# Kernel tuning notes

Hardware: AMD Instinct MI355X
Metric: run time of the kernel (lower is better)

Reference implementation:

```python
import jax, jax.numpy as jnp
import numpy as np

F_NODES = 16384   # number of function nodes
DEG = 8           # in-degree == out-degree per function node
E = F_NODES * DEG # edge-latent dimension (num edges)
B = 64            # batch
H = 16            # hidden_channels of each per-node MLP
LAYERS = 10       # GSNN layers (weights shared across layers)


def setup_inputs() -> dict:
    key = jax.random.key(0)
    k0, k1, k2, k3 = jax.random.split(key, 4)
    x0 = jax.random.normal(k0, (B, E), dtype=jnp.float32)
    # each edge has exactly one destination function node -> in_ixs is a permutation of edges
    in_ixs = jax.random.permutation(k1, E).reshape(F_NODES, DEG)
    # per-node 2-layer MLP weights: in_degree -> H -> out_degree
    W1 = jax.random.normal(k2, (F_NODES, H, DEG), dtype=jnp.float32) * (1.0 / np.sqrt(DEG))
    b1 = jnp.zeros((F_NODES, H), dtype=jnp.float32)
    W2 = jax.random.normal(k3, (F_NODES, DEG, H), dtype=jnp.float32) * (1.0 / np.sqrt(H))
    b2 = jnp.zeros((F_NODES, DEG), dtype=jnp.float32)
    return {"x0": x0, "W1": W1, "b1": b1, "W2": W2, "b2": b2, "in_ixs": in_ixs}


def reference(x0, W1, b1, W2, b2, in_ixs):
    # x0: [B, E] edge-latent input. Each layer: every function node gathers its
    # in-edges, applies its own small MLP, scatters to its out-edges; results are
    # summed into x_new and a residual x0 is added (GSNN.forward).
    x = x0
    for _ in range(LAYERS):
        g = x[:, in_ixs]                                   # [B, F, DEG] gather in-edge values
        h = jax.nn.elu(jnp.einsum('bfd,fhd->bfh', g, W1) + b1)  # [B, F, H]
        o = jnp.einsum('bfh,foh->bfo', h, W2) + b2         # [B, F, DEG]
        # out-edges of node f are the contiguous slots f*DEG:(f+1)*DEG (disjoint scatter)
        x = o.reshape(x0.shape) + x0                       # sum of node scatters + residual
    return x
```

## Files before the change

### kernel.cpp

```cpp
#include <hip/hip_runtime.h>
#include <math.h>

#define F_NODES 16384
#define DEG 8
#define E_TOT (F_NODES * DEG)
#define B 64
#define H 16
#define LAYERS 10

__global__ __launch_bounds__(256) void transpose_in_kernel(
    const float* __restrict__ x0, float* __restrict__ xT)
{
    __shared__ float tile[64 * 65];
    const int e0 = blockIdx.x * 64;
    const int c  = threadIdx.x & 63;
    const int r  = threadIdx.x >> 6;

    #pragma unroll
    for (int i = 0; i < 16; ++i) {
        const int b = r + i * 4;
        tile[c * 65 + b] = x0[(size_t)b * E_TOT + e0 + c];
    }
    __syncthreads();
    const int b = threadIdx.x & 63;
    #pragma unroll
    for (int i = 0; i < 16; ++i) {
        const int el = r + i * 4;
        xT[(size_t)(e0 + el) * B + b] = tile[el * 65 + b];
    }
}

__device__ __forceinline__ float fast_elu(float x)
{
    float e = __builtin_amdgcn_exp2f(x * 1.44269504088896340736f) - 1.0f;
    return x > 0.0f ? x : e;
}

#define NPW 2

template <bool FINAL>
__global__ __launch_bounds__(256) void layer_kernel(
    const float* __restrict__ xin,
    const float* __restrict__ x0T,
    const float* __restrict__ W1,
    const float* __restrict__ b1,
    const float* __restrict__ W2,
    const float* __restrict__ b2,
    const int*   __restrict__ in_ixs,
    float* __restrict__ xout)
{
    const int lane    = threadIdx.x & 63;
    const int wv      = threadIdx.x >> 6;
    const int wave_id = (int)blockIdx.x * 4 + wv;

    #pragma unroll
    for (int n = 0; n < NPW; ++n) {
        const int f = __builtin_amdgcn_readfirstlane(wave_id * NPW + n);

        const int* ixp = in_ixs + f * DEG;
        float g[DEG], r[DEG];
        const float* resp = x0T + (size_t)f * DEG * B + lane;
        #pragma unroll
        for (int d = 0; d < DEG; ++d) {
            const int ix = ixp[d];
            g[d] = xin[(size_t)ix * B + lane];
            r[d] = resp[d * B];
        }

        const float* w1  = W1 + f * (H * DEG);
        const float* bb1 = b1 + f * H;
        float h[H];
        #pragma unroll
        for (int j = 0; j < H; ++j) {
            float acc = bb1[j];
            #pragma unroll
            for (int d = 0; d < DEG; ++d)
                acc = fmaf(w1[j * DEG + d], g[d], acc);
            h[j] = fast_elu(acc);
        }

        const float* w2  = W2 + f * (DEG * H);
        const float* bb2 = b2 + f * DEG;
        float o[DEG];
        #pragma unroll
        for (int d = 0; d < DEG; ++d) {
            float acc = bb2[d];
            #pragma unroll
            for (int j = 0; j < H; ++j)
                acc = fmaf(w2[d * H + j], h[j], acc);
            o[d] = acc + r[d];
        }

        if (FINAL) {
            float4 v0 = make_float4(o[0], o[1], o[2], o[3]);
            float4 v1 = make_float4(o[4], o[5], o[6], o[7]);
            float4* dst = (float4*)(xout + (size_t)lane * E_TOT + f * DEG);
            dst[0] = v0;
            dst[1] = v1;
        } else {
            float* outp = xout + (size_t)f * DEG * B + lane;
            #pragma unroll
            for (int d = 0; d < DEG; ++d)
                outp[d * B] = o[d];
        }
    }
}

extern "C" void kernel_launch(void* const* d_in, const int* in_sizes, int n_in,
                              void* d_out, int out_size, void* d_ws, size_t ws_size,
                              hipStream_t stream)
{
    const float* x0     = (const float*)d_in[0];
    const float* W1     = (const float*)d_in[1];
    const float* b1     = (const float*)d_in[2];
    const float* W2     = (const float*)d_in[3];
    const float* b2     = (const float*)d_in[4];
    const int*   in_ixs = (const int*)d_in[5];
    float* out = (float*)d_out;

    const size_t NEL = (size_t)E_TOT * B;
    float* buf0 = (float*)d_ws;
    float* buf1 = buf0 + NEL;
    float* buf2 = buf1 + NEL;

    transpose_in_kernel<<<E_TOT / 64, 256, 0, stream>>>(x0, buf0);

    const int grid = F_NODES / (4 * NPW);
    const float* cur = buf0;
    float* nxt = buf1;
    for (int l = 0; l < LAYERS; ++l) {
        if (l == LAYERS - 1) {
            layer_kernel<true><<<grid, 256, 0, stream>>>(
                cur, buf0, W1, b1, W2, b2, in_ixs, out);
        } else {
            layer_kernel<false><<<grid, 256, 0, stream>>>(
                cur, buf0, W1, b1, W2, b2, in_ixs, nxt);
            cur = nxt;
            nxt = (cur == buf1) ? buf2 : buf1;
        }
    }
}
```

Before: 359.4 us.

## Store intermediate layers in consumer order so reads become sequential

Builds an inverse permutation of in_ixs once per call. Every non-final layer then scatters each node's outputs to the slots where their consuming node will read them. Later layers can read their inputs contiguously instead of through an index-dependent gather, which takes the dependent index load and the random reads off the load critical path. The random access moves to the stores, which do not stall the wave. It adds a small extra kernel and extra workspace for the inverse index array.

```diff
diff --git a/kernel.cpp b/kernel.cpp
--- a/kernel.cpp
+++ b/kernel.cpp
@@ -30,6 +30,13 @@
     }
 }
 
+__global__ __launch_bounds__(256) void build_inv_kernel(
+    const int* __restrict__ in_ixs, int* __restrict__ inv)
+{
+    const int k = blockIdx.x * 256 + threadIdx.x;
+    inv[in_ixs[k]] = k;
+}
+
 __device__ __forceinline__ float fast_elu(float x)
 {
     float e = __builtin_amdgcn_exp2f(x * 1.44269504088896340736f) - 1.0f;
@@ -38,7 +45,7 @@
 
 #define NPW 2
 
-template <bool FINAL>
+template <bool SEQ_IN, int OUT_MODE>
 __global__ __launch_bounds__(256) void layer_kernel(
     const float* __restrict__ xin,
     const float* __restrict__ x0T,
@@ -47,6 +54,7 @@
     const float* __restrict__ W2,
     const float* __restrict__ b2,
     const int*   __restrict__ in_ixs,
+    const int*   __restrict__ inv,
     float* __restrict__ xout)
 {
     const int lane    = threadIdx.x & 63;
@@ -57,14 +65,23 @@
     for (int n = 0; n < NPW; ++n) {
         const int f = __builtin_amdgcn_readfirstlane(wave_id * NPW + n);
 
-        const int* ixp = in_ixs + f * DEG;
         float g[DEG], r[DEG];
         const float* resp = x0T + (size_t)f * DEG * B + lane;
-        #pragma unroll
-        for (int d = 0; d < DEG; ++d) {
-            const int ix = ixp[d];
-            g[d] = xin[(size_t)ix * B + lane];
-            r[d] = resp[d * B];
+        if (SEQ_IN) {
+            const float* inp = xin + (size_t)f * DEG * B + lane;
+            #pragma unroll
+            for (int d = 0; d < DEG; ++d) {
+                g[d] = inp[d * B];
+                r[d] = resp[d * B];
+            }
+        } else {
+            const int* ixp = in_ixs + f * DEG;
+            #pragma unroll
+            for (int d = 0; d < DEG; ++d) {
+                const int ix = ixp[d];
+                g[d] = xin[(size_t)ix * B + lane];
+                r[d] = resp[d * B];
+            }
         }
 
         const float* w1  = W1 + f * (H * DEG);
@@ -91,17 +108,19 @@
             o[d] = acc + r[d];
         }
 
-        if (FINAL) {
+        if (OUT_MODE == 1) {
             float4 v0 = make_float4(o[0], o[1], o[2], o[3]);
             float4 v1 = make_float4(o[4], o[5], o[6], o[7]);
             float4* dst = (float4*)(xout + (size_t)lane * E_TOT + f * DEG);
             dst[0] = v0;
             dst[1] = v1;
         } else {
-            float* outp = xout + (size_t)f * DEG * B + lane;
+            const int* invp = inv + f * DEG;
             #pragma unroll
-            for (int d = 0; d < DEG; ++d)
-                outp[d * B] = o[d];
+            for (int d = 0; d < DEG; ++d) {
+                const int k = invp[d];
+                xout[(size_t)k * B + lane] = o[d];
+            }
         }
     }
 }
@@ -122,21 +141,25 @@
     float* buf0 = (float*)d_ws;
     float* buf1 = buf0 + NEL;
     float* buf2 = buf1 + NEL;
+    int*   inv  = (int*)(buf2 + NEL);
 
     transpose_in_kernel<<<E_TOT / 64, 256, 0, stream>>>(x0, buf0);
+    build_inv_kernel<<<E_TOT / 256, 256, 0, stream>>>(in_ixs, inv);
 
     const int grid = F_NODES / (4 * NPW);
-    const float* cur = buf0;
-    float* nxt = buf1;
-    for (int l = 0; l < LAYERS; ++l) {
-        if (l == LAYERS - 1) {
-            layer_kernel<true><<<grid, 256, 0, stream>>>(
-                cur, buf0, W1, b1, W2, b2, in_ixs, out);
-        } else {
-            layer_kernel<false><<<grid, 256, 0, stream>>>(
-                cur, buf0, W1, b1, W2, b2, in_ixs, nxt);
-            cur = nxt;
-            nxt = (cur == buf1) ? buf2 : buf1;
-        }
+
+    layer_kernel<false, 0><<<grid, 256, 0, stream>>>(
+        buf0, buf0, W1, b1, W2, b2, in_ixs, inv, buf1);
+
+    const float* cur = buf1;
+    float* nxt = buf2;
+    for (int l = 1; l < LAYERS - 1; ++l) {
+        layer_kernel<true, 0><<<grid, 256, 0, stream>>>(
+            cur, buf0, W1, b1, W2, b2, in_ixs, inv, nxt);
+        cur = nxt;
+        nxt = (cur == buf1) ? buf2 : buf1;
     }
+
+    layer_kernel<true, 1><<<grid, 256, 0, stream>>>(
+        cur, buf0, W1, b1, W2, b2, in_ixs, inv, out);
 }
```

Result: no change. 362.7 us (+0.9%).

## Fuse all layers into one cooperative kernel with scatter-side permutation and grid sync

Applied to the files above, without the earlier changes.

Replaces the ten per-layer launches with a single cooperative kernel of 256 blocks of 1024 threads. Layers are separated by grid-wide barriers. An inverse permutation of in_ixs is built up front, so each node scatters its outputs straight into the gather-order slots of the next layer and then reads its inputs contiguously. The residual x0 values are kept in registers across all layers. The costs are grid.sync overhead on each layer, scattered writes instead of scattered reads, and fewer resident waves (NPW=4 per wave) to hide latency.

```diff
diff --git a/kernel.cpp b/kernel.cpp
--- a/kernel.cpp
+++ b/kernel.cpp
@@ -1,5 +1,8 @@
 #include <hip/hip_runtime.h>
+#include <hip/hip_cooperative_groups.h>
 #include <math.h>
+
+namespace cg = cooperative_groups;
 
 #define F_NODES 16384
 #define DEG 8
@@ -7,6 +10,11 @@
 #define B 64
 #define H 16
 #define LAYERS 10
+
+#define NB  256
+#define TPB 1024
+#define NPB (F_NODES / NB)
+#define NPW (NPB / (TPB / 64))
 
 __global__ __launch_bounds__(256) void transpose_in_kernel(
     const float* __restrict__ x0, float* __restrict__ xT)
@@ -30,78 +38,115 @@
     }
 }
 
+__global__ __launch_bounds__(256) void build_inv_kernel(
+    const int* __restrict__ in_ixs, int* __restrict__ inv)
+{
+    const int k = blockIdx.x * 256 + threadIdx.x;
+    inv[in_ixs[k]] = k;
+}
+
 __device__ __forceinline__ float fast_elu(float x)
 {
     float e = __builtin_amdgcn_exp2f(x * 1.44269504088896340736f) - 1.0f;
     return x > 0.0f ? x : e;
 }
 
-#define NPW 2
-
-template <bool FINAL>
-__global__ __launch_bounds__(256) void layer_kernel(
-    const float* __restrict__ xin,
+__global__ __launch_bounds__(TPB, 4) void gsnn_fused(
     const float* __restrict__ x0T,
     const float* __restrict__ W1,
     const float* __restrict__ b1,
     const float* __restrict__ W2,
     const float* __restrict__ b2,
     const int*   __restrict__ in_ixs,
-    float* __restrict__ xout)
+    const int*   __restrict__ inv,
+    float* __restrict__ zA,
+    float* __restrict__ zB,
+    float* __restrict__ out)
 {
-    const int lane    = threadIdx.x & 63;
-    const int wv      = threadIdx.x >> 6;
-    const int wave_id = (int)blockIdx.x * 4 + wv;
+    cg::grid_group grid = cg::this_grid();
 
-    #pragma unroll
-    for (int n = 0; n < NPW; ++n) {
-        const int f = __builtin_amdgcn_readfirstlane(wave_id * NPW + n);
+    const int lane = threadIdx.x & 63;
+    const int wv   = threadIdx.x >> 6;
+    const int f0   = __builtin_amdgcn_readfirstlane(
+                        (int)blockIdx.x * NPB + wv * NPW);
 
-        const int* ixp = in_ixs + f * DEG;
-        float g[DEG], r[DEG];
-        const float* resp = x0T + (size_t)f * DEG * B + lane;
+    float r[NPW][DEG];
+    {
+        const float* rp = x0T + (size_t)f0 * DEG * B + lane;
         #pragma unroll
-        for (int d = 0; d < DEG; ++d) {
-            const int ix = ixp[d];
-            g[d] = xin[(size_t)ix * B + lane];
-            r[d] = resp[d * B];
+        for (int n = 0; n < NPW; ++n)
+            #pragma unroll
+            for (int d = 0; d < DEG; ++d)
+                r[n][d] = rp[(n * DEG + d) * B];
+    }
+
+    const float* zin  = nullptr;
+    float*       zout = zA;
+
+    for (int l = 0; l < LAYERS; ++l) {
+        float g[NPW][DEG];
+        if (l == 0) {
+            #pragma unroll
+            for (int n = 0; n < NPW; ++n) {
+                const int* ixp = in_ixs + (f0 + n) * DEG;
+                #pragma unroll
+                for (int d = 0; d < DEG; ++d)
+                    g[n][d] = x0T[(size_t)ixp[d] * B + lane];
+            }
+        } else {
+            const float* zp = zin + (size_t)f0 * DEG * B + lane;
+            #pragma unroll
+            for (int n = 0; n < NPW; ++n)
+                #pragma unroll
+                for (int d = 0; d < DEG; ++d)
+                    g[n][d] = zp[(n * DEG + d) * B];
         }
 
-        const float* w1  = W1 + f * (H * DEG);
-        const float* bb1 = b1 + f * H;
-        float h[H];
         #pragma unroll
-        for (int j = 0; j < H; ++j) {
-            float acc = bb1[j];
+        for (int n = 0; n < NPW; ++n) {
+            const int f = f0 + n;
+            const float* w1  = W1 + f * (H * DEG);
+            const float* bb1 = b1 + f * H;
+            float h[H];
             #pragma unroll
-            for (int d = 0; d < DEG; ++d)
-                acc = fmaf(w1[j * DEG + d], g[d], acc);
-            h[j] = fast_elu(acc);
+            for (int j = 0; j < H; ++j) {
+                float acc = bb1[j];
+                #pragma unroll
+                for (int d = 0; d < DEG; ++d)
+                    acc = fmaf(w1[j * DEG + d], g[n][d], acc);
+                h[j] = fast_elu(acc);
+            }
+
+            const float* w2  = W2 + f * (DEG * H);
+            const float* bb2 = b2 + f * DEG;
+            float o[DEG];
+            #pragma unroll
+            for (int d = 0; d < DEG; ++d) {
+                float acc = bb2[d];
+                #pragma unroll
+                for (int j = 0; j < H; ++j)
+                    acc = fmaf(w2[d * H + j], h[j], acc);
+                o[d] = acc + r[n][d];
+            }
+
+            if (l == LAYERS - 1) {
+                float4 v0 = make_float4(o[0], o[1], o[2], o[3]);
+                float4 v1 = make_float4(o[4], o[5], o[6], o[7]);
+                float4* dst = (float4*)(out + (size_t)lane * E_TOT + f * DEG);
+                dst[0] = v0;
+                dst[1] = v1;
+            } else {
+                const int* invp = inv + f * DEG;
+                #pragma unroll
+                for (int d = 0; d < DEG; ++d)
+                    zout[(size_t)invp[d] * B + lane] = o[d];
+            }
         }
 
-        const float* w2  = W2 + f * (DEG * H);
-        const float* bb2 = b2 + f * DEG;
-        float o[DEG];
-        #pragma unroll
-        for (int d = 0; d < DEG; ++d) {
-            float acc = bb2[d];
-            #pragma unroll
-            for (int j = 0; j < H; ++j)
-                acc = fmaf(w2[d * H + j], h[j], acc);
-            o[d] = acc + r[d];
-        }
-
-        if (FINAL) {
-            float4 v0 = make_float4(o[0], o[1], o[2], o[3]);
-            float4 v1 = make_float4(o[4], o[5], o[6], o[7]);
-            float4* dst = (float4*)(xout + (size_t)lane * E_TOT + f * DEG);
-            dst[0] = v0;
-            dst[1] = v1;
-        } else {
-            float* outp = xout + (size_t)f * DEG * B + lane;
-            #pragma unroll
-            for (int d = 0; d < DEG; ++d)
-                outp[d * B] = o[d];
+        if (l < LAYERS - 1) {
+            grid.sync();
+            zin  = zout;
+            zout = (zout == zA) ? zB : zA;
         }
     }
 }
@@ -120,23 +165,17 @@
 
     const size_t NEL = (size_t)E_TOT * B;
     float* buf0 = (float*)d_ws;
-    float* buf1 = buf0 + NEL;
-    float* buf2 = buf1 + NEL;
+    float* bufA = buf0 + NEL;
+    float* bufB = bufA + NEL;
+    int*   inv  = (int*)(bufB + NEL);
 
     transpose_in_kernel<<<E_TOT / 64, 256, 0, stream>>>(x0, buf0);
+    build_inv_kernel<<<E_TOT / 256, 256, 0, stream>>>(in_ixs, inv);
 
-    const int grid = F_NODES / (4 * NPW);
-    const float* cur = buf0;
-    float* nxt = buf1;
-    for (int l = 0; l < LAYERS; ++l) {
-        if (l == LAYERS - 1) {
-            layer_kernel<true><<<grid, 256, 0, stream>>>(
-                cur, buf0, W1, b1, W2, b2, in_ixs, out);
-        } else {
-            layer_kernel<false><<<grid, 256, 0, stream>>>(
-                cur, buf0, W1, b1, W2, b2, in_ixs, nxt);
-            cur = nxt;
-            nxt = (cur == buf1) ? buf2 : buf1;
-        }
-    }
+    void* args[] = {
+        (void*)&buf0, (void*)&W1, (void*)&b1, (void*)&W2, (void*)&b2,
+        (void*)&in_ixs, (void*)&inv, (void*)&bufA, (void*)&bufB, (void*)&out
+    };
+    hipLaunchCooperativeKernel((const void*)gsnn_fused,
+                               dim3(NB), dim3(TPB), args, 0, stream);
 }
```

Measured after the change: 738.4 us. 105% more time.

## Batch gathers for four nodes per wave upfront with nontemporal loads and stores

Applied to the files above, without the earlier changes.

Each wave now handles four function nodes and issues all gather and residual loads for them before any compute, raising memory-level parallelism. Blocks grow to 512 threads, with launch bounds that ask for at least four blocks resident. Activation loads and stores use nontemporal hints. The cost is higher register pressure from holding 64 gathered values per lane, which could lower occupancy or cause spills. The nontemporal hints may also hurt cache reuse of x0T and of the next layer's input.

```diff
diff --git a/kernel.cpp b/kernel.cpp
--- a/kernel.cpp
+++ b/kernel.cpp
@@ -7,6 +7,12 @@
 #define B 64
 #define H 16
 #define LAYERS 10
+
+#define WPB 8
+#define TPB (WPB * 64)
+#define NPW 4
+#define NODES_PER_BLOCK (WPB * NPW)
+#define GRID (F_NODES / NODES_PER_BLOCK)
 
 __global__ __launch_bounds__(256) void transpose_in_kernel(
     const float* __restrict__ x0, float* __restrict__ xT)
@@ -36,10 +42,8 @@
     return x > 0.0f ? x : e;
 }
 
-#define NPW 2
-
 template <bool FINAL>
-__global__ __launch_bounds__(256) void layer_kernel(
+__global__ __launch_bounds__(TPB, 4) void layer_kernel(
     const float* __restrict__ xin,
     const float* __restrict__ x0T,
     const float* __restrict__ W1,
@@ -49,24 +53,32 @@
     const int*   __restrict__ in_ixs,
     float* __restrict__ xout)
 {
-    const int lane    = threadIdx.x & 63;
-    const int wv      = threadIdx.x >> 6;
-    const int wave_id = (int)blockIdx.x * 4 + wv;
+    const int lane = threadIdx.x & 63;
+    const int wv   = threadIdx.x >> 6;
+    const int f0   = __builtin_amdgcn_readfirstlane(
+                        ((int)blockIdx.x * WPB + wv) * NPW);
+
+    float g[NPW][DEG];
+    float r[NPW][DEG];
+    #pragma unroll
+    for (int n = 0; n < NPW; ++n) {
+        const int* ixp = in_ixs + (f0 + n) * DEG;
+        #pragma unroll
+        for (int d = 0; d < DEG; ++d)
+            g[n][d] = __builtin_nontemporal_load(
+                          xin + (size_t)ixp[d] * B + lane);
+    }
+    #pragma unroll
+    for (int n = 0; n < NPW; ++n) {
+        const float* rp = x0T + (size_t)(f0 + n) * DEG * B + lane;
+        #pragma unroll
+        for (int d = 0; d < DEG; ++d)
+            r[n][d] = __builtin_nontemporal_load(rp + d * B);
+    }
 
     #pragma unroll
     for (int n = 0; n < NPW; ++n) {
-        const int f = __builtin_amdgcn_readfirstlane(wave_id * NPW + n);
-
-        const int* ixp = in_ixs + f * DEG;
-        float g[DEG], r[DEG];
-        const float* resp = x0T + (size_t)f * DEG * B + lane;
-        #pragma unroll
-        for (int d = 0; d < DEG; ++d) {
-            const int ix = ixp[d];
-            g[d] = xin[(size_t)ix * B + lane];
-            r[d] = resp[d * B];
-        }
-
+        const int f = f0 + n;
         const float* w1  = W1 + f * (H * DEG);
         const float* bb1 = b1 + f * H;
         float h[H];
@@ -75,7 +87,7 @@
             float acc = bb1[j];
             #pragma unroll
             for (int d = 0; d < DEG; ++d)
-                acc = fmaf(w1[j * DEG + d], g[d], acc);
+                acc = fmaf(w1[j * DEG + d], g[n][d], acc);
             h[j] = fast_elu(acc);
         }
 
@@ -88,7 +100,7 @@
             #pragma unroll
             for (int j = 0; j < H; ++j)
                 acc = fmaf(w2[d * H + j], h[j], acc);
-            o[d] = acc + r[d];
+            o[d] = acc + r[n][d];
         }
 
         if (FINAL) {
@@ -101,7 +113,7 @@
             float* outp = xout + (size_t)f * DEG * B + lane;
             #pragma unroll
             for (int d = 0; d < DEG; ++d)
-                outp[d * B] = o[d];
+                __builtin_nontemporal_store(o[d], outp + d * B);
         }
     }
 }
@@ -125,15 +137,14 @@
 
     transpose_in_kernel<<<E_TOT / 64, 256, 0, stream>>>(x0, buf0);
 
-    const int grid = F_NODES / (4 * NPW);
     const float* cur = buf0;
     float* nxt = buf1;
     for (int l = 0; l < LAYERS; ++l) {
         if (l == LAYERS - 1) {
-            layer_kernel<true><<<grid, 256, 0, stream>>>(
+            layer_kernel<true><<<GRID, TPB, 0, stream>>>(
                 cur, buf0, W1, b1, W2, b2, in_ixs, out);
         } else {
-            layer_kernel<false><<<grid, 256, 0, stream>>>(
+            layer_kernel<false><<<GRID, TPB, 0, stream>>>(
                 cur, buf0, W1, b1, W2, b2, in_ixs, nxt);
             cur = nxt;
             nxt = (cur == buf1) ? buf2 : buf1;
```

New measurement: 389.4 us. 1.08x slower.
